# Kernel optimization log

Hardware: AMD Instinct MI355X
Metric: run time of the kernel (lower is better)

The kernel has to match this reference:

```python
import jax, jax.numpy as jnp
import numpy as np

N_NODES = 100000
N_EDGES = 1600000
N_GRAPHS = 512
N_REL = 4
N_TYPES = 13
EMB = 128
HID = 128
BN_EPS = 1e-5
L2_EPS = 1e-12


def setup_inputs() -> dict:
    key = jax.random.key(0)
    ks = jax.random.split(key, 16)
    node_type = jax.random.randint(ks[0], (N_NODES,), 0, N_TYPES)
    x = jax.nn.one_hot(node_type, N_TYPES, dtype=jnp.float32)  # [N,13] one-hot
    edge_index = jax.random.randint(ks[1], (2, N_EDGES), 0, N_NODES)
    edge_type = jax.random.randint(ks[2], (N_EDGES,), 0, N_REL)
    batch = jnp.sort(jax.random.randint(ks[3], (N_NODES,), 0, N_GRAPHS))
    s = 0.05
    return {
        "x": x,
        "edge_index": edge_index,
        "edge_type": edge_type,
        "batch": batch,
        "emb": jax.random.normal(ks[4], (N_TYPES, EMB), jnp.float32) * s,
        "Wrel": jax.random.normal(ks[5], (2, N_REL, HID, HID), jnp.float32) * s,  # layer0 in=EMB==HID
        "Wroot": jax.random.normal(ks[6], (2, HID, HID), jnp.float32) * s,
        "conv_bias": jnp.zeros((2, HID), jnp.float32),
        "bn_gamma": jnp.ones((2, HID), jnp.float32),
        "bn_beta": jnp.zeros((2, HID), jnp.float32),
        "prelu_a": jnp.full((2,), 0.25, jnp.float32),
        "fc1_w": jax.random.normal(ks[7], (HID, 256), jnp.float32) * s,
        "fc1_b": jnp.zeros((256,), jnp.float32),
        "fc2_w": jax.random.normal(ks[8], (256, 128), jnp.float32) * s,
        "fc2_b": jnp.zeros((128,), jnp.float32),
        "out_w": jax.random.normal(ks[9], (128, 1), jnp.float32) * s,
        "out_b": jnp.zeros((1,), jnp.float32),
    }


def _rgcn_conv(h, Wrel, Wroot, bias, src, dst, edge_type):
    # PyG RGCNConv: out = h @ Wroot + bias + sum_r mean_{edges of rel r}(h_src @ W_r)
    n = h.shape[0]
    out = h @ Wroot + bias
    for r in range(N_REL):
        m = (edge_type == r).astype(h.dtype)  # [E]
        hr = h @ Wrel[r]                       # [N, dout]
        msg = hr[src] * m[:, None]             # gather + mask  [E, dout]
        num = jax.ops.segment_sum(msg, dst, num_segments=n)
        cnt = jax.ops.segment_sum(m, dst, num_segments=n)
        out = out + num / jnp.maximum(cnt, 1.0)[:, None]
    return out


def _batchnorm(h, gamma, beta):
    mu = jnp.mean(h, axis=0)
    var = jnp.mean((h - mu) ** 2, axis=0)  # biased var (training-mode BN)
    return (h - mu) * jax.lax.rsqrt(var + BN_EPS) * gamma + beta


def reference(x, edge_index, edge_type, batch, emb, Wrel, Wroot, conv_bias,
              bn_gamma, bn_beta, prelu_a, fc1_w, fc1_b, fc2_w, fc2_b, out_w, out_b):
    src, dst = edge_index[0], edge_index[1]
    idx = jnp.argmax(x, axis=1)         # torch.nonzero(one_hot)[1]
    h = emb[idx]                        # [N, EMB]
    for l in range(2):
        h = _rgcn_conv(h, Wrel[l], Wroot[l], conv_bias[l], src, dst, edge_type)
        h = _batchnorm(h, bn_gamma[l], bn_beta[l])
        h = jnp.where(h >= 0, h, prelu_a[l] * h)  # PReLU
        nrm = jnp.sqrt(jnp.sum(h * h, axis=1, keepdims=True))
        h = h / jnp.maximum(nrm, L2_EPS)          # F.normalize(p=2, dim=1)
    # global mean pool over graphs
    pooled = jax.ops.segment_sum(h, batch, num_segments=N_GRAPHS)
    cnt = jax.ops.segment_sum(jnp.ones((h.shape[0],), h.dtype), batch, num_segments=N_GRAPHS)
    g = pooled / jnp.maximum(cnt, 1.0)[:, None]   # [G, HID]
    g = jax.nn.relu(g @ fc1_w + fc1_b)
    g = jax.nn.relu(g @ fc2_w + fc2_b)
    return g @ out_w + out_b                      # [G, 1]
```

## Files before the change

kernel.cpp:

```cpp
#include <hip/hip_runtime.h>
#include <hip/hip_bf16.h>

#define NN 100000
#define NE 1600000
#define NG 512
#define CH3 65536
#define CHW 16384
#define NCH 2
#define BPC 128
#define ES 12500


typedef __attribute__((ext_vector_type(8))) short short8;
typedef __attribute__((ext_vector_type(4))) float float4v;


__device__ inline int lower_bound_dev(const int* __restrict__ a, int n, int v) {
    int lo = 0, hi = n;
    while (lo < hi) { int mid = (lo + hi) >> 1; if (a[mid] < v) lo = mid + 1; else hi = mid; }
    return lo;
}

__device__ inline unsigned short f2bf(float x) {
    unsigned u = __float_as_uint(x);
    unsigned r = (u + 0x7fffu + ((u >> 16) & 1u)) >> 16;
    return (unsigned short)r;
}

__device__ inline float bf2f(unsigned short h) {
    return __uint_as_float((unsigned)h << 16);
}


__global__ void node_type_kernel(const float* __restrict__ x, int* __restrict__ idx, int n) {
    int i = blockIdx.x * blockDim.x + threadIdx.x;
    if (i >= n) return;
    const float* row = x + (size_t)i * 13;
    int b = 0;
    #pragma unroll
    for (int t = 0; t < 13; ++t) if (row[t] > 0.5f) { b = t; }
    idx[i] = b;
}

__global__ void pack_src_type(const int* __restrict__ src, const int* __restrict__ ntype,
                              int* __restrict__ srcT) {
    int e = blockIdx.x * 256 + threadIdx.x;
    if (e >= NE) return;
    int s = src[e];
    srcT[e] = s | (ntype[s] << 17);
}


__global__ __launch_bounds__(256) void hist_kernel(const int* __restrict__ dst,
                                                   unsigned* __restrict__ partials) {
    __shared__ unsigned h[CHW];
    const int b = blockIdx.x, c = blockIdx.y;
    const int lo = c * CH3;
    for (int i = threadIdx.x; i < CHW; i += 256) h[i] = 0;
    __syncthreads();
    const int e0 = b * ES;
    const int e1 = (e0 + ES < NE) ? e0 + ES : NE;
    for (int e = e0 + threadIdx.x; e < e1; e += 256) {
        int k = dst[e] - lo;
        if (k >= 0 && k < CH3) atomicAdd(&h[k >> 2], 1u << ((k & 3) << 3));
    }
    __syncthreads();
    unsigned* out = partials + ((size_t)(c * BPC + b)) * CHW;
    for (int i = threadIdx.x; i < CHW; i += 256) out[i] = h[i];
}

__global__ void hist_reduce(unsigned* __restrict__ partials, int* __restrict__ counts) {
    const int c = blockIdx.y;
    const int i = blockIdx.x * 256 + threadIdx.x;
    size_t base = (size_t)c * BPC * CHW + i;
    unsigned r0 = 0, r1 = 0, r2 = 0, r3 = 0;
    #pragma unroll 4
    for (int b = 0; b < BPC; ++b) {
        unsigned t = partials[base + (size_t)b * CHW];
        partials[base + (size_t)b * CHW] = r0 | (r1 << 8) | (r2 << 16) | (r3 << 24);
        r0 += t & 0xffu; r1 += (t >> 8) & 0xffu; r2 += (t >> 16) & 0xffu; r3 += t >> 24;
    }
    int k0 = c * CH3 + 4 * i;
    if (k0 < NN)     counts[k0]     = (int)r0;
    if (k0 + 1 < NN) counts[k0 + 1] = (int)r1;
    if (k0 + 2 < NN) counts[k0 + 2] = (int)r2;
    if (k0 + 3 < NN) counts[k0 + 3] = (int)r3;
}

__global__ __launch_bounds__(256) void scan1(const int* __restrict__ counts, int* __restrict__ offs,
                                             int* __restrict__ bsums, int n) {
    __shared__ int wsum[4];
    const int base = blockIdx.x * 1024 + threadIdx.x * 4;
    int v[4]; int loc = 0;
    #pragma unroll
    for (int j = 0; j < 4; ++j) { int idx = base + j; v[j] = (idx < n) ? counts[idx] : 0; loc += v[j]; }
    const int lane = threadIdx.x & 63, wid = threadIdx.x >> 6;
    int sc = loc;
    #pragma unroll
    for (int o = 1; o < 64; o <<= 1) { int t = __shfl_up(sc, o, 64); if (lane >= o) sc += t; }
    if (lane == 63) wsum[wid] = sc;
    __syncthreads();
    int wbase = 0;
    for (int w = 0; w < wid; ++w) wbase += wsum[w];
    int run = wbase + sc - loc;
    #pragma unroll
    for (int j = 0; j < 4; ++j) { int idx = base + j; if (idx < n) offs[idx] = run; run += v[j]; }
    if (threadIdx.x == 255) bsums[blockIdx.x] = wbase + sc;
}

__global__ void scan2(int* __restrict__ bsums, int* __restrict__ offs, int nb, int n) {
    const int lane = threadIdx.x;
    int carry = 0;
    for (int base = 0; base < nb; base += 64) {
        int idx = base + lane;
        int v = (idx < nb) ? bsums[idx] : 0;
        int sc = v;
        #pragma unroll
        for (int o = 1; o < 64; o <<= 1) { int t = __shfl_up(sc, o, 64); if (lane >= o) sc += t; }
        if (idx < nb) bsums[idx] = carry + sc - v;
        int tot = __shfl(sc, 63, 64);
        carry += tot;
    }
    if (lane == 0) offs[n] = carry;
}

__global__ __launch_bounds__(256) void scan3(int* __restrict__ offs, const int* __restrict__ bsums, int n) {
    const int s = bsums[blockIdx.x];
    const int base = blockIdx.x * 1024 + threadIdx.x * 4;
    #pragma unroll
    for (int j = 0; j < 4; ++j) { int idx = base + j; if (idx < n) offs[idx] += s; }
}

__global__ __launch_bounds__(256) void place_kernel(const int* __restrict__ dst,
                                                    const int* __restrict__ et,
                                                    const int* __restrict__ srcT,
                                                    const int* __restrict__ offs,
                                                    const unsigned* __restrict__ partials,
                                                    int* __restrict__ sortedSrc) {
    __shared__ unsigned cur[CHW];
    const int b = blockIdx.x, c = blockIdx.y;
    const int lo = c * CH3;
    const unsigned* pb = partials + ((size_t)(c * BPC + b)) * CHW;
    for (int i = threadIdx.x; i < CHW; i += 256) cur[i] = pb[i];
    __syncthreads();
    const int e0 = b * ES;
    const int e1 = (e0 + ES < NE) ? e0 + ES : NE;
    for (int e = e0 + threadIdx.x; e < e1; e += 256) {
        int key = dst[e];
        int k = key - lo;
        if (k >= 0 && k < CH3) {
            int sh = (k & 3) << 3;
            unsigned old = atomicAdd(&cur[k >> 2], 1u << sh);
            int my = (int)((old >> sh) & 0xffu);
            int pos = offs[key] + my;
            sortedSrc[pos] = srcT[e] | (et[e] << 21);
        }
    }
}


__global__ __launch_bounds__(256) void relsort_hist(const int* __restrict__ sortedSrc,
                                                    const int* __restrict__ offs,
                                                    const int* __restrict__ ntype,
                                                    int* __restrict__ sorted2,
                                                    int* __restrict__ offs4,
                                                    unsigned short* __restrict__ A0) {
    __shared__ unsigned cnt[256][13];
    const int tid = threadIdx.x;
    const int n = blockIdx.x * 256 + tid;
    if (n >= NN) return;
    #pragma unroll
    for (int t = 0; t < 13; ++t) cnt[tid][t] = 0;
    const int o0 = offs[n], o1 = offs[n + 1];
    unsigned relc = 0;
    for (int i = o0; i < o1; ++i) {
        int v = sortedSrc[i];
        int ty = (v >> 17) & 15, r = v >> 21;
        cnt[tid][ty] += 1u << (r << 3);
        relc += 1u << (r << 3);
    }
    int b0 = o0;
    int b1 = b0 + (int)(relc & 0xffu);
    int b2 = b1 + (int)((relc >> 8) & 0xffu);
    int b3 = b2 + (int)((relc >> 16) & 0xffu);
    offs4[n * 4 + 0] = b0; offs4[n * 4 + 1] = b1;
    offs4[n * 4 + 2] = b2; offs4[n * 4 + 3] = b3;
    if (n == NN - 1) offs4[4 * NN] = o1;
    int c0 = b0, c1 = b1, c2 = b2, c3 = b3;
    for (int i = o0; i < o1; ++i) {
        int v = sortedSrc[i];
        int r = v >> 21;
        int pos;
        if (r == 0) pos = c0++;
        else if (r == 1) pos = c1++;
        else if (r == 2) pos = c2++;
        else pos = c3++;
        sorted2[pos] = v & 0x1ffff;
    }
    float inv[4];
    #pragma unroll
    for (int r = 0; r < 4; ++r) {
        unsigned c = (relc >> (r << 3)) & 0xffu;
        inv[r] = 1.0f / (float)(c > 0 ? c : 1);
    }
    const int myty = ntype[n];
    const int tile = n >> 4, l16 = n & 15;
    unsigned short* base = A0 + (size_t)tile * 1536 + l16 * 8;
    #pragma unroll
    for (int ks = 0; ks < 3; ++ks) {
        #pragma unroll
        for (int quad = 0; quad < 4; ++quad) {
            unsigned short vals[8];
            #pragma unroll
            for (int j = 0; j < 8; ++j) {
                int p = ks * 32 + quad * 8 + j;
                float v;
                if (p < 32) v = (p == myty) ? 1.0f : 0.0f;
                else {
                    int r = (p - 32) >> 4, tt = (p - 32) & 15;
                    v = (tt < 13) ? (float)((cnt[tid][tt] >> (r << 3)) & 0xffu) * inv[r] : 0.0f;
                }
                vals[j] = f2bf(v);
            }
            *(uint4*)(base + ks * 512 + quad * 128) = *(uint4*)vals;
        }
    }
}


__global__ void build_B0(const float* __restrict__ emb, const float* __restrict__ Wroot,
                         const float* __restrict__ Wrel, unsigned short* __restrict__ B0f,
                         float* __restrict__ bnSums) {
    if (blockIdx.x < 8) bnSums[blockIdx.x * 256 + threadIdx.x] = 0.f;
    int i = blockIdx.x * 256 + threadIdx.x;
    if (i >= 12288) return;
    int j = i & 7;
    int lane = (i >> 3) & 63;
    int t = (i >> 9) & 7;
    int ks = i >> 12;
    int n = t * 16 + (lane & 15);
    int p = ks * 32 + (lane >> 4) * 8 + j;
    float val = 0.f;
    if (p < 32) {
        if (p < 13) {
            const float* er = emb + (size_t)p * 128;
            const float* wc = Wroot + n;
            float acc = 0.f;
            for (int k = 0; k < 128; ++k) acc += er[k] * wc[(size_t)k * 128];
            val = acc;
        }
    } else {
        int r = (p - 32) >> 4, tt = (p - 32) & 15;
        if (tt < 13) {
            const float* er = emb + (size_t)tt * 128;
            const float* wc = Wrel + ((size_t)r * 128) * 128 + n;
            float acc = 0.f;
            for (int k = 0; k < 128; ++k) acc += er[k] * wc[(size_t)k * 128];
            val = acc;
        }
    }
    B0f[i] = f2bf(val);
}


__global__ void build_Bf1(const float* __restrict__ Wroot, const float* __restrict__ Wrel,
                          unsigned short* __restrict__ Bf, float* __restrict__ bnSums) {
    if (blockIdx.x < 8) bnSums[blockIdx.x * 256 + threadIdx.x] = 0.f;
    int i = blockIdx.x * 256 + threadIdx.x;
    if (i >= 81920) return;
    int j = i & 7;
    int lane = (i >> 3) & 63;
    int t = (i >> 9) & 7;
    int ks = (i >> 12) & 3;
    int kc = i >> 14;
    int n = t * 16 + (lane & 15);
    int kcol = j * 16 + ks * 4 + (lane >> 4);
    float w;
    if (kc == 0) w = Wroot[16384 + (size_t)kcol * 128 + n];
    else {
        int r = kc - 1;
        w = Wrel[(((size_t)(4 + r) * 128) + kcol) * 128 + n];
    }
    Bf[i] = f2bf(w);
}


__global__ __launch_bounds__(256) void gemm0_mfma(const unsigned short* __restrict__ A0,
                                                  const unsigned short* __restrict__ B0f,
                                                  const float* __restrict__ bias,
                                                  unsigned short* __restrict__ Cb,
                                                  float* __restrict__ bnSums, int M) {
    __shared__ float sred[2][4][128];
    const int tid = threadIdx.x;
    const int wv = tid >> 6, lane = tid & 63;
    const int l16 = lane & 15, quad = lane >> 4;
    const int rowbase = blockIdx.x * 128 + wv * 32;
    const int tmax = (M >> 4) - 1;
    int tile0 = blockIdx.x * 8 + wv * 2; if (tile0 > tmax) tile0 = tmax;
    int tile1 = tile0 + 1;               if (tile1 > tmax) tile1 = tmax;

    float4v acc[2][8];
    #pragma unroll
    for (int t = 0; t < 8; ++t) {
        float bv = bias[t * 16 + l16];
        float4v av = {bv, bv, bv, bv};
        acc[0][t] = av; acc[1][t] = av;
    }

    const unsigned short* bl = B0f + lane * 8;
    const unsigned short* F0 = A0 + (size_t)tile0 * 1536 + quad * 128 + l16 * 8;
    const unsigned short* F1 = A0 + (size_t)tile1 * 1536 + quad * 128 + l16 * 8;
    #pragma unroll
    for (int ks = 0; ks < 3; ++ks) {
        short8 af0 = *(const short8*)(F0 + ks * 512);
        short8 af1 = *(const short8*)(F1 + ks * 512);
        const unsigned short* bp = bl + ((ks * 8) << 9);
        #pragma unroll
        for (int t = 0; t < 8; ++t) {
            short8 bf = *(const short8*)(bp + (t << 9));
            acc[0][t] = __builtin_amdgcn_mfma_f32_16x16x32_bf16(af0, bf, acc[0][t], 0, 0, 0);
            acc[1][t] = __builtin_amdgcn_mfma_f32_16x16x32_bf16(af1, bf, acc[1][t], 0, 0, 0);
        }
    }

    #pragma unroll
    for (int h = 0; h < 2; ++h) {
        #pragma unroll
        for (int rg = 0; rg < 4; ++rg) {
            int rr = rowbase + h * 16 + quad * 4 + rg;
            if (rr < M) {
                unsigned short v[8];
                #pragma unroll
                for (int t = 0; t < 8; ++t) v[t] = f2bf(acc[h][t][rg]);
                *(uint4*)(Cb + (size_t)rr * 128 + l16 * 8) = *(uint4*)v;
            }
        }
    }
    float s[8], q[8];
    #pragma unroll
    for (int t = 0; t < 8; ++t) {
        s[t] = 0.f; q[t] = 0.f;
        #pragma unroll
        for (int h = 0; h < 2; ++h) {
            #pragma unroll
            for (int rg = 0; rg < 4; ++rg) {
                int rr = rowbase + h * 16 + quad * 4 + rg;
                if (rr < M) { float v = acc[h][t][rg]; s[t] += v; q[t] += v * v; }
            }
        }
    }
    #pragma unroll
    for (int t = 0; t < 8; ++t) {
        s[t] += __shfl_down(s[t], 32, 64); q[t] += __shfl_down(q[t], 32, 64);
        s[t] += __shfl_down(s[t], 16, 64); q[t] += __shfl_down(q[t], 16, 64);
    }
    if (lane < 16) {
        #pragma unroll
        for (int t = 0; t < 8; ++t) {
            sred[0][wv][t * 16 + l16] = s[t];
            sred[1][wv][t * 16 + l16] = q[t];
        }
    }
    __syncthreads();
    if (tid < 128) {
        float S = sred[0][0][tid] + sred[0][1][tid] + sred[0][2][tid] + sred[0][3][tid];
        float Q = sred[1][0][tid] + sred[1][1][tid] + sred[1][2][tid] + sred[1][3][tid];
        float* bnS = bnSums + ((blockIdx.x & 7) << 8);
        unsafeAtomicAdd(bnS + tid, S);
        unsafeAtomicAdd(bnS + 128 + tid, Q);
    }
}


__global__ __launch_bounds__(256) void gather_gemm1(const unsigned short* __restrict__ hbf,
                                                    const int* __restrict__ sorted2,
                                                    const int* __restrict__ offs4,
                                                    const unsigned short* __restrict__ Bf,
                                                    const float* __restrict__ bias,
                                                    unsigned short* __restrict__ Cb,
                                                    float* __restrict__ bnSums) {
    __shared__ unsigned short rootL[2048];
    __shared__ unsigned short aggL[8192];
    const int tid = threadIdx.x;
    const int tile = blockIdx.x;
    {
        const int l16g = tid >> 4;
        const int cidx = tid & 15;
        const int c8 = cidx << 3;
        const int n = tile * 16 + l16g;
        const int pu = cidx * 16 + (l16g ^ cidx);
        uint4 ru = *(const uint4*)(hbf + (size_t)n * 128 + c8);
        *(uint4*)(rootL + pu * 8) = ru;

        const unsigned short* hb = hbf + c8;
        const int ob = n * 4;
        auto acc8 = [](float* a, uint4 u) {
            a[0] += __uint_as_float(u.x << 16); a[1] += __uint_as_float(u.x & 0xffff0000u);
            a[2] += __uint_as_float(u.y << 16); a[3] += __uint_as_float(u.y & 0xffff0000u);
            a[4] += __uint_as_float(u.z << 16); a[5] += __uint_as_float(u.z & 0xffff0000u);
            a[6] += __uint_as_float(u.w << 16); a[7] += __uint_as_float(u.w & 0xffff0000u);
        };
        #pragma unroll
        for (int r = 0; r < 4; ++r) {
            const int i0 = offs4[ob + r];
            const int i1 = offs4[ob + r + 1];
            float aA[8], aB[8];
            #pragma unroll
            for (int j = 0; j < 8; ++j) { aA[j] = 0.f; aB[j] = 0.f; }
            int i = i0;
            for (; i + 4 <= i1; i += 4) {
                int s0 = sorted2[i], s1 = sorted2[i + 1];
                int s2 = sorted2[i + 2], s3 = sorted2[i + 3];
                uint4 u0 = *(const uint4*)(hb + (size_t)s0 * 128);
                uint4 u1 = *(const uint4*)(hb + (size_t)s1 * 128);
                uint4 u2 = *(const uint4*)(hb + (size_t)s2 * 128);
                uint4 u3 = *(const uint4*)(hb + (size_t)s3 * 128);
                acc8(aA, u0); acc8(aB, u1); acc8(aA, u2); acc8(aB, u3);
            }
            if (i + 2 <= i1) {
                int s0 = sorted2[i], s1 = sorted2[i + 1];
                uint4 u0 = *(const uint4*)(hb + (size_t)s0 * 128);
                uint4 u1 = *(const uint4*)(hb + (size_t)s1 * 128);
                acc8(aA, u0); acc8(aB, u1);
                i += 2;
            }
            if (i < i1) {
                int s0 = sorted2[i];
                uint4 u0 = *(const uint4*)(hb + (size_t)s0 * 128);
                acc8(aA, u0);
            }
            const int cnt = i1 - i0;
            const float inv = 1.0f / (float)(cnt > 0 ? cnt : 1);
            unsigned short v[8];
            #pragma unroll
            for (int j = 0; j < 8; ++j) v[j] = f2bf((aA[j] + aB[j]) * inv);
            *(uint4*)(aggL + r * 2048 + pu * 8) = *(uint4*)v;
        }
    }
    __syncthreads();

    const int wv = tid >> 6, lane = tid & 63;
    const int l16 = lane & 15, quad = lane >> 4;
    const int t0 = wv << 1;
    float4v acc0, acc1;
    {
        float b0v = bias[t0 * 16 + l16];
        float b1v = bias[(t0 + 1) * 16 + l16];
        float4v a0v = {b0v, b0v, b0v, b0v};
        float4v a1v = {b1v, b1v, b1v, b1v};
        acc0 = a0v; acc1 = a1v;
    }
    const unsigned short* bl = Bf + lane * 8;
    #pragma unroll
    for (int kc = 0; kc < 5; ++kc) {
        const unsigned short* Abase = (kc == 0) ? rootL : (aggL + (kc - 1) * 2048);
        #pragma unroll
        for (int ks = 0; ks < 4; ++ks) {
            const int C = ks * 4 + quad;
            const int p = C * 16 + (l16 ^ C);
            short8 af = *(const short8*)(Abase + p * 8);
            const unsigned short* bp = bl + (((kc * 4 + ks) * 8 + t0) << 9);
            short8 b0 = *(const short8*)(bp);
            short8 b1 = *(const short8*)(bp + 512);
            acc0 = __builtin_amdgcn_mfma_f32_16x16x32_bf16(af, b0, acc0, 0, 0, 0);
            acc1 = __builtin_amdgcn_mfma_f32_16x16x32_bf16(af, b1, acc1, 0, 0, 0);
        }
    }
    const int rowbase = tile * 16;
    #pragma unroll
    for (int rg = 0; rg < 4; ++rg) {
        int rr = rowbase + quad * 4 + rg;
        unsigned pk = (unsigned)f2bf(acc0[rg]) | ((unsigned)f2bf(acc1[rg]) << 16);
        *(unsigned*)(Cb + (size_t)rr * 128 + l16 * 8 + t0) = pk;
    }
    float s0 = 0.f, q0 = 0.f, s1 = 0.f, q1 = 0.f;
    #pragma unroll
    for (int rg = 0; rg < 4; ++rg) {
        float v0 = acc0[rg], v1 = acc1[rg];
        s0 += v0; q0 += v0 * v0; s1 += v1; q1 += v1 * v1;
    }
    s0 += __shfl_down(s0, 32, 64); q0 += __shfl_down(q0, 32, 64);
    s1 += __shfl_down(s1, 32, 64); q1 += __shfl_down(q1, 32, 64);
    s0 += __shfl_down(s0, 16, 64); q0 += __shfl_down(q0, 16, 64);
    s1 += __shfl_down(s1, 16, 64); q1 += __shfl_down(q1, 16, 64);
    if (lane < 16) {
        float* bnS = bnSums + ((tile & 7) << 8);
        unsafeAtomicAdd(bnS + t0 * 16 + l16, s0);
        unsafeAtomicAdd(bnS + 128 + t0 * 16 + l16, q0);
        unsafeAtomicAdd(bnS + (t0 + 1) * 16 + l16, s1);
        unsafeAtomicAdd(bnS + 128 + (t0 + 1) * 16 + l16, q1);
    }
}


__global__ void bn_finalize(const float* __restrict__ bnSums, float* __restrict__ fin,
                            float* __restrict__ g0zero, int n) {
    const int c = threadIdx.x;
    if (g0zero) g0zero[blockIdx.x * 128 + c] = 0.f;
    if (blockIdx.x != 0) return;
    float s = 0.f, q = 0.f;
    #pragma unroll
    for (int j = 0; j < 8; ++j) { s += bnSums[j * 256 + c]; q += bnSums[j * 256 + 128 + c]; }
    const float invn = 1.0f / (float)n;
    float mu = s * invn;
    float var = q * invn - mu * mu; if (var < 0.f) var = 0.f;
    fin[c] = mu;
    fin[128 + c] = rsqrtf(var + 1e-5f);
}


__global__ __launch_bounds__(256) void bn_apply_kernel(const unsigned short* __restrict__ Cb,
                                unsigned short* __restrict__ hbf,
                                const float* __restrict__ fin,
                                const float* __restrict__ gamma, const float* __restrict__ beta,
                                const float* __restrict__ prelu_a, int layer) {
    const int tid = threadIdx.x;
    const int row = blockIdx.x * 16 + (tid >> 4);
    const int li = tid & 15;
    const int p8 = li << 3;
    const float a = prelu_a[layer];
    uint4 u = *(const uint4*)(Cb + (size_t)row * 128 + p8);
    float v[8];
    v[0] = __uint_as_float(u.x << 16); v[1] = __uint_as_float(u.x & 0xffff0000u);
    v[2] = __uint_as_float(u.y << 16); v[3] = __uint_as_float(u.y & 0xffff0000u);
    v[4] = __uint_as_float(u.z << 16); v[5] = __uint_as_float(u.z & 0xffff0000u);
    v[6] = __uint_as_float(u.w << 16); v[7] = __uint_as_float(u.w & 0xffff0000u);
    float t[8]; float ss = 0.f;
    #pragma unroll
    for (int j = 0; j < 8; ++j) {
        int cc = j * 16 + li;
        float tv = (v[j] - fin[cc]) * fin[128 + cc] * gamma[cc] + beta[cc];
        tv = (tv >= 0.f) ? tv : a * tv;
        t[j] = tv; ss += tv * tv;
    }
    ss += __shfl_xor(ss, 1, 64);
    ss += __shfl_xor(ss, 2, 64);
    ss += __shfl_xor(ss, 4, 64);
    ss += __shfl_xor(ss, 8, 64);
    const float scale = 1.0f / fmaxf(sqrtf(ss), 1e-12f);
    unsigned short o[8];
    #pragma unroll
    for (int j = 0; j < 8; ++j) o[j] = f2bf(t[j] * scale);
    *(uint4*)(hbf + (size_t)row * 128 + p8) = *(uint4*)o;
}


__global__ __launch_bounds__(256) void bn_apply_pool(const unsigned short* __restrict__ Cb,
                                const float* __restrict__ fin,
                                const float* __restrict__ gamma, const float* __restrict__ beta,
                                const float* __restrict__ prelu_a,
                                const int* __restrict__ batch,
                                float* __restrict__ g0) {
    __shared__ float P[16][128];
    __shared__ int gids[16];
    const int tid = threadIdx.x;
    const int r16 = tid >> 4;
    const int li = tid & 15;
    const int row = blockIdx.x * 16 + r16;
    const int p8 = li << 3;
    if (li == 0) gids[r16] = batch[row];
    const float a = prelu_a[1];
    uint4 u = *(const uint4*)(Cb + (size_t)row * 128 + p8);
    float v[8];
    v[0] = __uint_as_float(u.x << 16); v[1] = __uint_as_float(u.x & 0xffff0000u);
    v[2] = __uint_as_float(u.y << 16); v[3] = __uint_as_float(u.y & 0xffff0000u);
    v[4] = __uint_as_float(u.z << 16); v[5] = __uint_as_float(u.z & 0xffff0000u);
    v[6] = __uint_as_float(u.w << 16); v[7] = __uint_as_float(u.w & 0xffff0000u);
    float t[8]; float ss = 0.f;
    #pragma unroll
    for (int j = 0; j < 8; ++j) {
        int cc = j * 16 + li;
        float tv = (v[j] - fin[cc]) * fin[128 + cc] * gamma[cc] + beta[cc];
        tv = (tv >= 0.f) ? tv : a * tv;
        t[j] = tv; ss += tv * tv;
    }
    ss += __shfl_xor(ss, 1, 64);
    ss += __shfl_xor(ss, 2, 64);
    ss += __shfl_xor(ss, 4, 64);
    ss += __shfl_xor(ss, 8, 64);
    const float scale = 1.0f / fmaxf(sqrtf(ss), 1e-12f);
    #pragma unroll
    for (int j = 0; j < 8; ++j) P[r16][p8 + j] = t[j] * scale;
    __syncthreads();
    if (tid < 128) {
        int cur = gids[0];
        float run = 0.f;
        #pragma unroll
        for (int rr = 0; rr < 16; ++rr) {
            int g = gids[rr];
            if (g != cur) {
                unsafeAtomicAdd(&g0[(size_t)cur * 128 + tid], run);
                run = 0.f; cur = g;
            }
            run += P[rr][tid];
        }
        unsafeAtomicAdd(&g0[(size_t)cur * 128 + tid], run);
    }
}


__global__ void fc1_kernel(const float* __restrict__ g, const float* __restrict__ w,
                           const float* __restrict__ b, const int* __restrict__ batch,
                           float* __restrict__ o) {
    const int row = blockIdx.x;
    const int j = threadIdx.x;
    const int lo = lower_bound_dev(batch, NN, row);
    const int hi = lower_bound_dev(batch, NN, row + 1);
    const int c = hi - lo;
    const float invc = 1.0f / (float)(c > 0 ? c : 1);
    float acc = 0.f;
    #pragma unroll 8
    for (int k = 0; k < 128; ++k) {
        int lk = (k & 7) * 16 + (k >> 3);
        acc += g[row * 128 + k] * w[lk * 256 + j];
    }
    o[row * 256 + j] = fmaxf(acc * invc + b[j], 0.f);
}

__global__ void fc2_kernel(const float* __restrict__ g, const float* __restrict__ w,
                           const float* __restrict__ b, float* __restrict__ o) {
    const int row = blockIdx.x;
    const int j = threadIdx.x;
    float acc = b[j];
    #pragma unroll 8
    for (int k = 0; k < 256; ++k) acc += g[row * 256 + k] * w[k * 128 + j];
    o[row * 128 + j] = fmaxf(acc, 0.f);
}

__global__ void fco_kernel(const float* __restrict__ g, const float* __restrict__ w,
                           const float* __restrict__ b, float* __restrict__ o) {
    const int row = blockIdx.x * blockDim.x + threadIdx.x;
    if (row >= NG) return;
    float acc = b[0];
    #pragma unroll 8
    for (int k = 0; k < 128; ++k) acc += g[row * 128 + k] * w[k];
    o[row] = acc;
}


extern "C" void kernel_launch(void* const* d_in, const int* in_sizes, int n_in,
                              void* d_out, int out_size, void* d_ws, size_t ws_size,
                              hipStream_t stream) {
    const float* x      = (const float*)d_in[0];
    const int*   eidx   = (const int*)d_in[1];
    const int*   etype  = (const int*)d_in[2];
    const int*   batch  = (const int*)d_in[3];
    const float* emb    = (const float*)d_in[4];
    const float* Wrel   = (const float*)d_in[5];
    const float* Wroot  = (const float*)d_in[6];
    const float* cbias  = (const float*)d_in[7];
    const float* gamma  = (const float*)d_in[8];
    const float* beta   = (const float*)d_in[9];
    const float* prelua = (const float*)d_in[10];
    const float* fc1w   = (const float*)d_in[11];
    const float* fc1b   = (const float*)d_in[12];
    const float* fc2w   = (const float*)d_in[13];
    const float* fc2b   = (const float*)d_in[14];
    const float* outw   = (const float*)d_in[15];
    const float* outb   = (const float*)d_in[16];
    float* out = (float*)d_out;

    const int* src = eidx;
    const int* dst = eidx + NE;

    char* p = (char*)d_ws;
    auto alloc = [&](size_t bytes) { char* r = p; p += (bytes + 255) & ~(size_t)255; return r; };
    unsigned short* hbf   = (unsigned short*)alloc((size_t)NN * 128 * 2);
    unsigned short* Cb    = (unsigned short*)alloc((size_t)NN * 128 * 2);
    char*  scratch   = (char*)alloc((size_t)24 << 20);
    int*   sortedSrc = (int*)alloc((size_t)NE * 4);
    int*   sorted2   = (int*)alloc((size_t)NE * 4);
    int*   srcT      = (int*)alloc((size_t)NE * 4);
    int*   offs      = (int*)alloc((size_t)(NN + 1) * 4);
    int*   offs4     = (int*)alloc((size_t)(4 * NN + 1) * 4);
    int*   bsums     = (int*)alloc(1024);
    int*   ntype     = (int*)alloc((size_t)NN * 4);
    unsigned short* Bf1 = (unsigned short*)alloc((size_t)81920 * 2);
    unsigned short* B0f = (unsigned short*)alloc((size_t)12288 * 2);
    float* bnSums  = (float*)alloc(2048 * 4);
    float* bnFin   = (float*)alloc(256 * 4);
    float* g0      = (float*)alloc((size_t)NG * 128 * 4);
    float* g1      = (float*)alloc((size_t)NG * 256 * 4);
    float* g2      = (float*)alloc((size_t)NG * 128 * 4);

    unsigned* partials = (unsigned*)scratch;
    unsigned short* A0 = (unsigned short*)scratch;

    const int NBLK = (NN + 1023) / 1024;

    node_type_kernel<<<(NN + 255) / 256, 256, 0, stream>>>(x, ntype, NN);
    pack_src_type<<<(NE + 255) / 256, 256, 0, stream>>>(src, ntype, srcT);

    hist_kernel<<<dim3(BPC, NCH), 256, 0, stream>>>(dst, partials);
    hist_reduce<<<dim3(CHW / 256, NCH), 256, 0, stream>>>(partials, offs);
    scan1<<<NBLK, 256, 0, stream>>>(offs, offs, bsums, NN);
    scan2<<<1, 64, 0, stream>>>(bsums, offs, NBLK, NN);
    scan3<<<NBLK, 256, 0, stream>>>(offs, bsums, NN);
    place_kernel<<<dim3(BPC, NCH), 256, 0, stream>>>(dst, etype, srcT, offs, partials, sortedSrc);

    relsort_hist<<<(NN + 255) / 256, 256, 0, stream>>>(sortedSrc, offs, ntype,
                                                       sorted2, offs4, A0);

    build_B0<<<48, 256, 0, stream>>>(emb, Wroot, Wrel, B0f, bnSums);
    gemm0_mfma<<<(NN + 127) / 128, 256, 0, stream>>>(A0, B0f, cbias, Cb, bnSums, NN);
    bn_finalize<<<1, 128, 0, stream>>>(bnSums, bnFin, (float*)nullptr, NN);
    bn_apply_kernel<<<NN / 16, 256, 0, stream>>>(Cb, hbf, bnFin, gamma, beta, prelua, 0);

    build_Bf1<<<320, 256, 0, stream>>>(Wroot, Wrel, Bf1, bnSums);
    gather_gemm1<<<NN / 16, 256, 0, stream>>>(hbf, sorted2, offs4, Bf1, cbias + 128, Cb, bnSums);
    bn_finalize<<<512, 128, 0, stream>>>(bnSums, bnFin, g0, NN);
    bn_apply_pool<<<NN / 16, 256, 0, stream>>>(Cb, bnFin, gamma + 128, beta + 128,
                                               prelua, batch, g0);

    fc1_kernel<<<NG, 256, 0, stream>>>(g0, fc1w, fc1b, batch, g1);
    fc2_kernel<<<NG, 128, 0, stream>>>(g1, fc2w, fc2b, g2);
    fco_kernel<<<2, 256, 0, stream>>>(g2, outw, outb, out);
}
```

Baseline: 380.8 us.

## Drop per-relation re-sort; split relations with masked accumulators during gather

Removes the second, per-relation scatter that produced sorted2 and offs4 in the histogram kernel. The layer-1 gather now walks the dst-sorted edge list once and adds each neighbour row into one of four relation accumulators through 0/1 masked FMAs, counting edges per relation on the fly. This saves a 1.6M-entry write and re-read plus the offs4 array, and lowers serial work in relsort. In exchange the gather does four times the FMA work per edge and holds 32 extra accumulator registers, which may reduce occupancy.

```diff
diff --git a/kernel.cpp b/kernel.cpp
--- a/kernel.cpp
+++ b/kernel.cpp
@@ -159,12 +159,10 @@
 }
 
 
-__global__ __launch_bounds__(256) void relsort_hist(const int* __restrict__ sortedSrc,
-                                                    const int* __restrict__ offs,
-                                                    const int* __restrict__ ntype,
-                                                    int* __restrict__ sorted2,
-                                                    int* __restrict__ offs4,
-                                                    unsigned short* __restrict__ A0) {
+__global__ __launch_bounds__(256) void hist_A0(const int* __restrict__ sortedSrc,
+                                               const int* __restrict__ offs,
+                                               const int* __restrict__ ntype,
+                                               unsigned short* __restrict__ A0) {
     __shared__ unsigned cnt[256][13];
     const int tid = threadIdx.x;
     const int n = blockIdx.x * 256 + tid;
@@ -178,24 +176,6 @@
         int ty = (v >> 17) & 15, r = v >> 21;
         cnt[tid][ty] += 1u << (r << 3);
         relc += 1u << (r << 3);
-    }
-    int b0 = o0;
-    int b1 = b0 + (int)(relc & 0xffu);
-    int b2 = b1 + (int)((relc >> 8) & 0xffu);
-    int b3 = b2 + (int)((relc >> 16) & 0xffu);
-    offs4[n * 4 + 0] = b0; offs4[n * 4 + 1] = b1;
-    offs4[n * 4 + 2] = b2; offs4[n * 4 + 3] = b3;
-    if (n == NN - 1) offs4[4 * NN] = o1;
-    int c0 = b0, c1 = b1, c2 = b2, c3 = b3;
-    for (int i = o0; i < o1; ++i) {
-        int v = sortedSrc[i];
-        int r = v >> 21;
-        int pos;
-        if (r == 0) pos = c0++;
-        else if (r == 1) pos = c1++;
-        else if (r == 2) pos = c2++;
-        else pos = c3++;
-        sorted2[pos] = v & 0x1ffff;
     }
     float inv[4];
     #pragma unroll
@@ -373,8 +353,8 @@
 
 
 __global__ __launch_bounds__(256) void gather_gemm1(const unsigned short* __restrict__ hbf,
-                                                    const int* __restrict__ sorted2,
-                                                    const int* __restrict__ offs4,
+                                                    const int* __restrict__ sortedSrc,
+                                                    const int* __restrict__ offs,
                                                     const unsigned short* __restrict__ Bf,
                                                     const float* __restrict__ bias,
                                                     unsigned short* __restrict__ Cb,
@@ -393,49 +373,68 @@
         *(uint4*)(rootL + pu * 8) = ru;
 
         const unsigned short* hb = hbf + c8;
-        const int ob = n * 4;
-        auto acc8 = [](float* a, uint4 u) {
-            a[0] += __uint_as_float(u.x << 16); a[1] += __uint_as_float(u.x & 0xffff0000u);
-            a[2] += __uint_as_float(u.y << 16); a[3] += __uint_as_float(u.y & 0xffff0000u);
-            a[4] += __uint_as_float(u.z << 16); a[5] += __uint_as_float(u.z & 0xffff0000u);
-            a[6] += __uint_as_float(u.w << 16); a[7] += __uint_as_float(u.w & 0xffff0000u);
+        const int o0 = offs[n], o1 = offs[n + 1];
+
+        float a0[8], a1[8], a2[8], a3[8];
+        #pragma unroll
+        for (int j = 0; j < 8; ++j) { a0[j] = 0.f; a1[j] = 0.f; a2[j] = 0.f; a3[j] = 0.f; }
+        float c0 = 0.f, c1 = 0.f, c2 = 0.f, c3 = 0.f;
+
+        auto body = [&](int v, uint4 u) {
+            int r = v >> 21;
+            float f[8];
+            f[0] = __uint_as_float(u.x << 16); f[1] = __uint_as_float(u.x & 0xffff0000u);
+            f[2] = __uint_as_float(u.y << 16); f[3] = __uint_as_float(u.y & 0xffff0000u);
+            f[4] = __uint_as_float(u.z << 16); f[5] = __uint_as_float(u.z & 0xffff0000u);
+            f[6] = __uint_as_float(u.w << 16); f[7] = __uint_as_float(u.w & 0xffff0000u);
+            float m0 = (r == 0) ? 1.f : 0.f, m1 = (r == 1) ? 1.f : 0.f;
+            float m2 = (r == 2) ? 1.f : 0.f, m3 = (r == 3) ? 1.f : 0.f;
+            c0 += m0; c1 += m1; c2 += m2; c3 += m3;
+            #pragma unroll
+            for (int j = 0; j < 8; ++j) {
+                a0[j] = fmaf(m0, f[j], a0[j]);
+                a1[j] = fmaf(m1, f[j], a1[j]);
+                a2[j] = fmaf(m2, f[j], a2[j]);
+                a3[j] = fmaf(m3, f[j], a3[j]);
+            }
         };
-        #pragma unroll
-        for (int r = 0; r < 4; ++r) {
-            const int i0 = offs4[ob + r];
-            const int i1 = offs4[ob + r + 1];
-            float aA[8], aB[8];
-            #pragma unroll
-            for (int j = 0; j < 8; ++j) { aA[j] = 0.f; aB[j] = 0.f; }
-            int i = i0;
-            for (; i + 4 <= i1; i += 4) {
-                int s0 = sorted2[i], s1 = sorted2[i + 1];
-                int s2 = sorted2[i + 2], s3 = sorted2[i + 3];
-                uint4 u0 = *(const uint4*)(hb + (size_t)s0 * 128);
-                uint4 u1 = *(const uint4*)(hb + (size_t)s1 * 128);
-                uint4 u2 = *(const uint4*)(hb + (size_t)s2 * 128);
-                uint4 u3 = *(const uint4*)(hb + (size_t)s3 * 128);
-                acc8(aA, u0); acc8(aB, u1); acc8(aA, u2); acc8(aB, u3);
-            }
-            if (i + 2 <= i1) {
-                int s0 = sorted2[i], s1 = sorted2[i + 1];
-                uint4 u0 = *(const uint4*)(hb + (size_t)s0 * 128);
-                uint4 u1 = *(const uint4*)(hb + (size_t)s1 * 128);
-                acc8(aA, u0); acc8(aB, u1);
-                i += 2;
-            }
-            if (i < i1) {
-                int s0 = sorted2[i];
-                uint4 u0 = *(const uint4*)(hb + (size_t)s0 * 128);
-                acc8(aA, u0);
-            }
-            const int cnt = i1 - i0;
-            const float inv = 1.0f / (float)(cnt > 0 ? cnt : 1);
+
+        int i = o0;
+        for (; i + 4 <= o1; i += 4) {
+            int v0 = sortedSrc[i], v1 = sortedSrc[i + 1];
+            int v2 = sortedSrc[i + 2], v3 = sortedSrc[i + 3];
+            uint4 u0 = *(const uint4*)(hb + (size_t)(v0 & 0x1ffff) * 128);
+            uint4 u1 = *(const uint4*)(hb + (size_t)(v1 & 0x1ffff) * 128);
+            uint4 u2 = *(const uint4*)(hb + (size_t)(v2 & 0x1ffff) * 128);
+            uint4 u3 = *(const uint4*)(hb + (size_t)(v3 & 0x1ffff) * 128);
+            body(v0, u0); body(v1, u1); body(v2, u2); body(v3, u3);
+        }
+        if (i + 2 <= o1) {
+            int v0 = sortedSrc[i], v1 = sortedSrc[i + 1];
+            uint4 u0 = *(const uint4*)(hb + (size_t)(v0 & 0x1ffff) * 128);
+            uint4 u1 = *(const uint4*)(hb + (size_t)(v1 & 0x1ffff) * 128);
+            body(v0, u0); body(v1, u1);
+            i += 2;
+        }
+        if (i < o1) {
+            int v0 = sortedSrc[i];
+            uint4 u0 = *(const uint4*)(hb + (size_t)(v0 & 0x1ffff) * 128);
+            body(v0, u0);
+        }
+
+        const float i0 = 1.f / fmaxf(c0, 1.f), i1 = 1.f / fmaxf(c1, 1.f);
+        const float i2 = 1.f / fmaxf(c2, 1.f), i3 = 1.f / fmaxf(c3, 1.f);
+        unsigned short* bp = aggL + pu * 8;
+        auto pack = [&](float* a, float inv, unsigned short* dp) {
             unsigned short v[8];
             #pragma unroll
-            for (int j = 0; j < 8; ++j) v[j] = f2bf((aA[j] + aB[j]) * inv);
-            *(uint4*)(aggL + r * 2048 + pu * 8) = *(uint4*)v;
-        }
+            for (int j = 0; j < 8; ++j) v[j] = f2bf(a[j] * inv);
+            *(uint4*)dp = *(uint4*)v;
+        };
+        pack(a0, i0, bp);
+        pack(a1, i1, bp + 2048);
+        pack(a2, i2, bp + 4096);
+        pack(a3, i3, bp + 6144);
     }
     __syncthreads();
 
@@ -669,10 +668,8 @@
     unsigned short* Cb    = (unsigned short*)alloc((size_t)NN * 128 * 2);
     char*  scratch   = (char*)alloc((size_t)24 << 20);
     int*   sortedSrc = (int*)alloc((size_t)NE * 4);
-    int*   sorted2   = (int*)alloc((size_t)NE * 4);
     int*   srcT      = (int*)alloc((size_t)NE * 4);
     int*   offs      = (int*)alloc((size_t)(NN + 1) * 4);
-    int*   offs4     = (int*)alloc((size_t)(4 * NN + 1) * 4);
     int*   bsums     = (int*)alloc(1024);
     int*   ntype     = (int*)alloc((size_t)NN * 4);
     unsigned short* Bf1 = (unsigned short*)alloc((size_t)81920 * 2);
@@ -698,8 +695,7 @@
     scan3<<<NBLK, 256, 0, stream>>>(offs, bsums, NN);
     place_kernel<<<dim3(BPC, NCH), 256, 0, stream>>>(dst, etype, srcT, offs, partials, sortedSrc);
 
-    relsort_hist<<<(NN + 255) / 256, 256, 0, stream>>>(sortedSrc, offs, ntype,
-                                                       sorted2, offs4, A0);
+    hist_A0<<<(NN + 255) / 256, 256, 0, stream>>>(sortedSrc, offs, ntype, A0);
 
     build_B0<<<48, 256, 0, stream>>>(emb, Wroot, Wrel, B0f, bnSums);
     gemm0_mfma<<<(NN + 127) / 128, 256, 0, stream>>>(A0, B0f, cbias, Cb, bnSums, NN);
@@ -707,7 +703,7 @@
     bn_apply_kernel<<<NN / 16, 256, 0, stream>>>(Cb, hbf, bnFin, gamma, beta, prelua, 0);
 
     build_Bf1<<<320, 256, 0, stream>>>(Wroot, Wrel, Bf1, bnSums);
-    gather_gemm1<<<NN / 16, 256, 0, stream>>>(hbf, sorted2, offs4, Bf1, cbias + 128, Cb, bnSums);
+    gather_gemm1<<<NN / 16, 256, 0, stream>>>(hbf, sortedSrc, offs, Bf1, cbias + 128, Cb, bnSums);
     bn_finalize<<<512, 128, 0, stream>>>(bnSums, bnFin, g0, NN);
     bn_apply_pool<<<NN / 16, 256, 0, stream>>>(Cb, bnFin, gamma + 128, beta + 128,
                                                prelua, batch, g0);
```

New measurement: 374.8 us. No clear change (-1.6%).
